# Optimization experiments

Hardware: AMD Instinct MI355X
Metric: run time of the kernel (lower is better)

Reference implementation:

```python
import jax, jax.numpy as jnp
import numpy as np

D_MODEL = 64     # input_dim // 4
D_INNER = 128    # expand * d_model
D_STATE = 16
D_CONV = 4
DT_RANK = 4      # ceil(d_model / 16)
EPS = 1e-5


def layernorm(x, g, b):
    m = x.mean(-1, keepdims=True)
    v = x.var(-1, keepdims=True)
    return (x - m) * jax.lax.rsqrt(v + EPS) * g + b


def mamba(u, W_in, W_conv, b_conv, W_xproj, W_dt, b_dt, A_log, Dp, W_out):
    # u: [B, L, d_model]
    B, L, _ = u.shape
    xz = u @ W_in.T                              # [B, L, 2*d_inner]
    xi, z = xz[..., :D_INNER], xz[..., D_INNER:]
    # depthwise causal conv1d over L
    xp = jnp.pad(xi, ((0, 0), (D_CONV - 1, 0), (0, 0)))
    xc = b_conv + sum(xp[:, k:k + L, :] * W_conv[:, k] for k in range(D_CONV))
    xc = jax.nn.silu(xc)                         # [B, L, d_inner]
    proj = xc @ W_xproj.T                        # [B, L, dt_rank + 2*d_state]
    dtp = proj[..., :DT_RANK]
    Bm = proj[..., DT_RANK:DT_RANK + D_STATE]    # [B, L, d_state]
    Cm = proj[..., DT_RANK + D_STATE:]           # [B, L, d_state]
    dt = jax.nn.softplus(dtp @ W_dt.T + b_dt)    # [B, L, d_inner]
    A = -jnp.exp(A_log)                          # [d_inner, d_state]
    dA = jnp.exp(dt[..., None] * A)              # [B, L, d_inner, d_state]
    dBx = (dt * xc)[..., None] * Bm[:, :, None, :]

    def step(h, t):
        dA_t, dBx_t, C_t = t
        h = dA_t * h + dBx_t                     # [B, d_inner, d_state]
        return h, jnp.einsum('bds,bs->bd', h, C_t)

    h0 = jnp.zeros((B, D_INNER, D_STATE), u.dtype)
    _, ys = jax.lax.scan(step, h0, (dA.transpose(1, 0, 2, 3),
                                    dBx.transpose(1, 0, 2, 3),
                                    Cm.transpose(1, 0, 2)))
    y = ys.transpose(1, 0, 2) + Dp * xc          # [B, L, d_inner]
    y = y * jax.nn.silu(z)
    return y @ W_out.T                           # [B, L, d_model]


def _forward(x, x1, x2, x3, g1, be1, g2, be2, g3, be3, g4, be4, skip_scale,
             W_in, W_conv, b_conv, W_xproj, W_dt, b_dt, A_log, D, W_out):
    Bb, C = x.shape[:2]
    img_dims = x2.shape[2:]
    mparams = (W_in, W_conv, b_conv, W_xproj, W_dt, b_dt, A_log, D, W_out)

    def branch(inp, g, b):
        xf = inp.reshape(Bb, C, -1).transpose(0, 2, 1)   # [B, L, C]
        xn = layernorm(xf, g, b)
        return mamba(xn, *mparams) + skip_scale * xn

    x_mamba = jnp.concatenate([branch(x, g1, be1), branch(x1, g2, be2),
                               branch(x2, g3, be3), branch(x3, g4, be4)], axis=2)
    out = x_mamba.transpose(0, 2, 1).reshape(Bb, 4 * C, *img_dims)
    return out


def setup_inputs():
    key = jax.random.key(0)
    ks = jax.random.split(key, 12)
    f = lambda k, shp, s=1.0: jax.random.normal(k, shp, dtype=jnp.float32) * s
    inp = {
        'x': f(ks[0], (8, 64, 32, 32)),
        'x1': f(ks[1], (8, 64, 32, 32)),
        'x2': f(ks[2], (8, 64, 32, 32)),
        'x3': f(ks[3], (8, 64, 32, 32)),
        'g1': jnp.ones(64), 'be1': jnp.zeros(64),
        'g2': jnp.ones(64), 'be2': jnp.zeros(64),
        'g3': jnp.ones(64), 'be3': jnp.zeros(64),
        'g4': jnp.ones(64), 'be4': jnp.zeros(64),
        'skip_scale': jnp.ones((1,), jnp.float32),
        'W_in': f(ks[4], (2 * D_INNER, D_MODEL), 0.1),
        'W_conv': f(ks[5], (D_INNER, D_CONV), 0.3),
        'b_conv': jnp.zeros(D_INNER),
        'W_xproj': f(ks[6], (DT_RANK + 2 * D_STATE, D_INNER), 0.1),
        'W_dt': f(ks[7], (D_INNER, DT_RANK), 0.1),
        'b_dt': f(ks[8], (D_INNER,), 0.1),
        'A_log': jnp.log(jnp.tile(jnp.arange(1, D_STATE + 1, dtype=jnp.float32), (D_INNER, 1))),
        'D': jnp.ones(D_INNER),
        'W_out': f(ks[9], (D_MODEL, D_INNER), 0.1),
    }
    return inp


def reference(x, x1, x2, x3, g1, be1, g2, be2, g3, be3, g4, be4, skip_scale,
              W_in, W_conv, b_conv, W_xproj, W_dt, b_dt, A_log, D, W_out):
    return _forward(x, x1, x2, x3, g1, be1, g2, be2, g3, be3, g4, be4, skip_scale,
                    W_in, W_conv, b_conv, W_xproj, W_dt, b_dt, A_log, D, W_out)
```

## Files before the change

kernel.cpp:

```cpp
#include <hip/hip_runtime.h>
#include <hip/hip_bf16.h>

#define L2E 1.4426950408889634f
#define LN2 0.6931471805599453f

__device__ __forceinline__ float fexp2(float x) { return __builtin_amdgcn_exp2f(x); }
__device__ __forceinline__ float flog2(float x) { return __builtin_amdgcn_logf(x); }
__device__ __forceinline__ int uniform(int x) { return __builtin_amdgcn_readfirstlane(x); }
__device__ __forceinline__ float sigmoidf_(float v) { return 1.f / (1.f + fexp2(-v * L2E)); }
__device__ __forceinline__ float softplusf_(float t) {
    return (t > 20.f) ? t : LN2 * flog2(1.f + fexp2(t * L2E));
}

constexpr size_t O_M   = 0;
constexpr size_t O_RS  = 32768;
constexpr size_t O_G   = 65536;
constexpr size_t O_Z   = 4259840;
constexpr size_t O_XC  = 8454144;
constexpr size_t O_BM  = 12648448;
constexpr size_t O_CM  = 13172736;
constexpr size_t O_HP  = 13828096;
constexpr size_t O_DT  = 18022400;
constexpr size_t O_DX  = 22216704;

__global__ __launch_bounds__(256) void k1_ln_inproj(
    const float* __restrict__ x0, const float* __restrict__ x1,
    const float* __restrict__ x2, const float* __restrict__ x3,
    const float* __restrict__ win,
    const float* __restrict__ g1, const float* __restrict__ be1,
    const float* __restrict__ g2, const float* __restrict__ be2,
    const float* __restrict__ g3, const float* __restrict__ be3,
    const float* __restrict__ g4, const float* __restrict__ be4,
    float* __restrict__ ws)
{
    __shared__ float sX[64 * 68];
    __shared__ float sW[64 * 68];
    __shared__ float sM[64], sR[64];
    int bid = blockIdx.x;
    int seq = bid >> 4, pb = bid & 15;
    int branch = seq >> 3, b = seq & 7;
    int tid = threadIdx.x;
    int lane = tid & 63;
    int wq = uniform(tid >> 6);
    const float* xin = (branch==0)?x0:(branch==1)?x1:(branch==2)?x2:x3;
    const float* gam = (branch==0)?g1:(branch==1)?g2:(branch==2)?g3:g4;
    const float* bet = (branch==0)?be1:(branch==1)?be2:(branch==2)?be3:be4;
    const float* xb = xin + (size_t)b * 65536;

#pragma unroll
    for (int r = 0; r < 16; ++r) {
        int row = r * 4 + wq;
        sX[row * 68 + lane] = xb[(size_t)row * 1024 + pb * 64 + lane];
    }
    __syncthreads();
    if (tid < 64) {
        float sum = 0.f, sq = 0.f;
#pragma unroll
        for (int c = 0; c < 64; ++c) {
            float v = sX[c * 68 + tid];
            sum += v; sq += v * v;
        }
        float mean = sum * (1.f/64.f);
        float var  = sq * (1.f/64.f) - mean * mean;
        float rs   = rsqrtf(var + 1e-5f);
        sM[tid] = mean; sR[tid] = rs;
        ws[O_M  + (size_t)seq * 1024 + pb * 64 + tid] = mean;
        ws[O_RS + (size_t)seq * 1024 + pb * 64 + tid] = rs;
    }
    __syncthreads();
#pragma unroll
    for (int r = 0; r < 16; ++r) {
        int c = r * 4 + wq;
        float v = sX[c * 68 + lane];
        sX[c * 68 + lane] = (v - sM[lane]) * sR[lane] * gam[c] + bet[c];
    }
    __syncthreads();

    int jt = tid >> 4, pt = tid & 15;
    int p0 = pb * 64 + pt * 4;
    float* xi = ws + O_G + (size_t)seq * 131072;
    float* zz = ws + O_Z + (size_t)seq * 131072;

    for (int jb = 0; jb < 4; ++jb) {
#pragma unroll
        for (int r = 0; r < 16; ++r) {
            int row = r * 4 + wq;
            sW[lane * 68 + row] = win[(size_t)(jb * 64 + row) * 64 + lane];
        }
        __syncthreads();
        float acc[4][4];
#pragma unroll
        for (int i = 0; i < 4; ++i)
#pragma unroll
            for (int j = 0; j < 4; ++j) acc[i][j] = 0.f;
        for (int c = 0; c < 64; ++c) {
            float4 wv = *(const float4*)&sW[c * 68 + jt * 4];
            float4 xv = *(const float4*)&sX[c * 68 + pt * 4];
            float w[4] = {wv.x, wv.y, wv.z, wv.w};
            float x[4] = {xv.x, xv.y, xv.z, xv.w};
#pragma unroll
            for (int i = 0; i < 4; ++i)
#pragma unroll
                for (int j = 0; j < 4; ++j) acc[i][j] += w[i] * x[j];
        }
#pragma unroll
        for (int ji = 0; ji < 4; ++ji) {
            int j = jb * 64 + jt * 4 + ji;
            float4 v = make_float4(acc[ji][0], acc[ji][1], acc[ji][2], acc[ji][3]);
            if (j < 128) *(float4*)&xi[(size_t)j * 1024 + p0] = v;
            else         *(float4*)&zz[(size_t)(j - 128) * 1024 + p0] = v;
        }
        __syncthreads();
    }
}

__global__ __launch_bounds__(256) void k2_conv_proj(
    const float* __restrict__ wconv, const float* __restrict__ bconv,
    const float* __restrict__ wxp,
    const float* __restrict__ wdt, const float* __restrict__ bdt,
    const float* __restrict__ alog,
    float* __restrict__ ws)
{
    __shared__ float buf[17408];
    __shared__ __align__(16) float sDtp4[64 * 4];
    __shared__ float sB5[64 * 20];
    float* sX  = buf;
    float* sWr = buf + 8704;
    float* sDt = buf + 8704;

    int bid = blockIdx.x;
    int seq = bid >> 4, ptile = bid & 15;
    int tid = threadIdx.x;
    int lane = tid & 63;
    int wq = uniform(tid >> 6);
    int p0 = ptile * 64;
    int p  = p0 + lane;
    int j0 = wq * 9;

    const float* xirow = ws + O_G  + (size_t)seq * 131072;
    float*       xcrow = ws + O_XC + (size_t)seq * 131072;

#pragma unroll 4
    for (int r = 0; r < 32; ++r) {
        int d = r * 4 + wq;
        const float* row = xirow + (size_t)d * 1024;
        int gp = p0 - 3 + lane;
        sX[d * 68 + lane] = (gp >= 0) ? row[gp] : 0.f;
        if (lane < 3) sX[d * 68 + 64 + lane] = row[p0 + 61 + lane];
    }
#pragma unroll
    for (int jj = 0; jj < 9; ++jj) {
#pragma unroll
        for (int half = 0; half < 2; ++half) {
            int d = half * 64 + lane;
            sWr[(wq * 128 + d) * 12 + jj] = wxp[(size_t)(j0 + jj) * 128 + d];
        }
    }
    __syncthreads();

#pragma unroll 2
    for (int dd = 0; dd < 32; ++dd) {
        int d = wq * 32 + dd;
        float4 wc = *(const float4*)&wconv[d * 4];
        float v = bconv[d];
        float* rowl = &sX[d * 68];
        v += rowl[lane + 0] * wc.x;
        v += rowl[lane + 1] * wc.y;
        v += rowl[lane + 2] * wc.z;
        v += rowl[lane + 3] * wc.w;
        v = v * sigmoidf_(v);
        xcrow[(size_t)d * 1024 + p] = v;
        rowl[lane + 3] = v;
    }
    __syncthreads();

    float acc[9];
#pragma unroll
    for (int jj = 0; jj < 9; ++jj) acc[jj] = 0.f;
#pragma unroll 4
    for (int d = 0; d < 128; ++d) {
        float xcv = sX[d * 68 + 3 + lane];
        const float* wr = &sWr[(wq * 128 + d) * 12];
        float4 wA = *(const float4*)wr;
        float4 wB = *(const float4*)(wr + 4);
        float  w8 = wr[8];
        acc[0] += wA.x * xcv; acc[1] += wA.y * xcv;
        acc[2] += wA.z * xcv; acc[3] += wA.w * xcv;
        acc[4] += wB.x * xcv; acc[5] += wB.y * xcv;
        acc[6] += wB.z * xcv; acc[7] += wB.w * xcv;
        acc[8] += w8 * xcv;
    }

    float* Bm = ws + O_BM + (size_t)seq * 16384;
    float* Cm = ws + O_CM + (size_t)seq * 16384;
#pragma unroll
    for (int jj = 0; jj < 9; ++jj) {
        int j = j0 + jj;
        if (j < 4) continue;
        float t = acc[jj];
        if (j < 20) { Bm[(size_t)(j - 4) * 1024 + p] = t; sB5[lane * 20 + (j - 4)] = t; }
        else        Cm[(size_t)(j - 20) * 1024 + p] = t;
    }
    if (wq == 0)
        *(float4*)&sDtp4[lane * 4] = make_float4(acc[0], acc[1], acc[2], acc[3]);
    __syncthreads();

    float* dtg = ws + O_DT + (size_t)seq * 131072;
    float* dxg = ws + O_DX + (size_t)seq * 131072;
    float4 qv = *(const float4*)&sDtp4[lane * 4];
#pragma unroll 4
    for (int dd = 0; dd < 32; ++dd) {
        int d = wq * 32 + dd;
        float4 wv = *(const float4*)&wdt[d * 4];
        float t = bdt[d] + qv.x*wv.x + qv.y*wv.y + qv.z*wv.z + qv.w*wv.w;
        float dt = softplusf_(t);
        float xc = sX[d * 68 + 3 + lane];
        float dx = dt * xc;
        dtg[(size_t)d * 1024 + p] = dt;
        dxg[(size_t)d * 1024 + p] = dx;
        sDt[d * 68 + lane] = dt;
        sX [d * 68 + lane] = dx;
    }
    __syncthreads();

    {
        int dA = tid >> 2;
        int dB = dA + 64;
        int s05 = (tid & 3) * 4;
        float a2[8];
        {
            float4 a0 = *(const float4*)(alog + dA * 16 + s05);
            float4 a1 = *(const float4*)(alog + dB * 16 + s05);
            a2[0] = -fexp2(a0.x * L2E) * L2E; a2[1] = -fexp2(a0.y * L2E) * L2E;
            a2[2] = -fexp2(a0.z * L2E) * L2E; a2[3] = -fexp2(a0.w * L2E) * L2E;
            a2[4] = -fexp2(a1.x * L2E) * L2E; a2[5] = -fexp2(a1.y * L2E) * L2E;
            a2[6] = -fexp2(a1.z * L2E) * L2E; a2[7] = -fexp2(a1.w * L2E) * L2E;
        }
        float* hp0 = ws + O_HP + (size_t)(seq * 32 + ptile * 2) * 4096;
#pragma unroll
        for (int cc = 0; cc < 2; ++cc) {
            const float* dtA = &sDt[dA * 68 + cc * 32];
            const float* dtB = &sDt[dB * 68 + cc * 32];
            const float* dxA = &sX [dA * 68 + cc * 32];
            const float* dxB = &sX [dB * 68 + cc * 32];
            float h[8];
#pragma unroll
            for (int i = 0; i < 8; ++i) h[i] = 0.f;
            float sdtA = 0.f, sdtB = 0.f;
            for (int q4 = 0; q4 < 8; ++q4) {
                float4 t0 = *(const float4*)&dtA[q4 * 4];
                float4 t1 = *(const float4*)&dtB[q4 * 4];
                float4 x0 = *(const float4*)&dxA[q4 * 4];
                float4 x1 = *(const float4*)&dxB[q4 * 4];
                float t0a[4] = {t0.x, t0.y, t0.z, t0.w};
                float t1a[4] = {t1.x, t1.y, t1.z, t1.w};
                float x0a[4] = {x0.x, x0.y, x0.z, x0.w};
                float x1a[4] = {x1.x, x1.y, x1.z, x1.w};
#pragma unroll
                for (int k = 0; k < 4; ++k) {
                    int li = q4 * 4 + k;
                    float4 Bv = *(const float4*)&sB5[(cc * 32 + li) * 20 + s05];
                    float bv[4] = {Bv.x, Bv.y, Bv.z, Bv.w};
                    float dt0 = t0a[k], dt1 = t1a[k];
                    float dx0 = x0a[k], dx1 = x1a[k];
                    sdtA += dt0; sdtB += dt1;
#pragma unroll
                    for (int ss = 0; ss < 4; ++ss) {
                        float e0 = fexp2(dt0 * a2[ss]);
                        h[ss] = e0 * h[ss] + dx0 * bv[ss];
                        float e1 = fexp2(dt1 * a2[4 + ss]);
                        h[4 + ss] = e1 * h[4 + ss] + dx1 * bv[ss];
                    }
                }
            }
            float* hp = hp0 + cc * 4096;
            *(float4*)&hp[dA * 16 + s05] = make_float4(
                fexp2(a2[0] * sdtA), fexp2(a2[1] * sdtA),
                fexp2(a2[2] * sdtA), fexp2(a2[3] * sdtA));
            *(float4*)&hp[dB * 16 + s05] = make_float4(
                fexp2(a2[4] * sdtB), fexp2(a2[5] * sdtB),
                fexp2(a2[6] * sdtB), fexp2(a2[7] * sdtB));
            *(float4*)&hp[2048 + dA * 16 + s05] = make_float4(h[0], h[1], h[2], h[3]);
            *(float4*)&hp[2048 + dB * 16 + s05] = make_float4(h[4], h[5], h[6], h[7]);
        }
    }
}

__device__ __forceinline__ void a2_preload(const float* alog, int d0, int s0, float* a2)
{
    float4 a0 = *(const float4*)(alog + d0 * 16 + s0);
    float4 a1 = *(const float4*)(alog + (d0 + 1) * 16 + s0);
    a2[0] = -fexp2(a0.x * L2E) * L2E; a2[1] = -fexp2(a0.y * L2E) * L2E;
    a2[2] = -fexp2(a0.z * L2E) * L2E; a2[3] = -fexp2(a0.w * L2E) * L2E;
    a2[4] = -fexp2(a1.x * L2E) * L2E; a2[5] = -fexp2(a1.y * L2E) * L2E;
    a2[6] = -fexp2(a1.z * L2E) * L2E; a2[7] = -fexp2(a1.w * L2E) * L2E;
}

__global__ __launch_bounds__(256) void k3b_compose(float* __restrict__ ws)
{
    int seq = blockIdx.x >> 3, dg = blockIdx.x & 7;
    int idx = dg * 256 + threadIdx.x;
    float h = 0.f;
    float* hpb = ws + O_HP + (size_t)seq * 32 * 4096;
    float P = hpb[idx];
    float E = hpb[2048 + idx];
    for (int c = 0; c < 32; ++c) {
        float* hp = hpb + (size_t)c * 4096;
        float Pn = 0.f, En = 0.f;
        if (c < 31) { Pn = hp[4096 + idx]; En = hp[4096 + 2048 + idx]; }
        hp[idx] = h;
        h = P * h + E;
        P = Pn; E = En;
    }
}

__global__ __launch_bounds__(256) void k3cd(
    const float* __restrict__ alog,
    const float* __restrict__ x0, const float* __restrict__ x1,
    const float* __restrict__ x2, const float* __restrict__ x3,
    const float* __restrict__ g1, const float* __restrict__ be1,
    const float* __restrict__ g2, const float* __restrict__ be2,
    const float* __restrict__ g3, const float* __restrict__ be3,
    const float* __restrict__ g4, const float* __restrict__ be4,
    const float* __restrict__ dpar, const float* __restrict__ woutp,
    const float* __restrict__ skipp, float* __restrict__ ws,
    float* __restrict__ out)
{
    __shared__ __align__(16) float sY[128 * 36];
    __shared__ __align__(16) float sB[32 * 16];
    __shared__ __align__(16) float sC[32 * 16];
    int bid = blockIdx.x;
    int seq = bid >> 5, ch = bid & 31;
    int branch = seq >> 3, b = seq & 7;
    int lb = ch * 32;
    int tid = threadIdx.x;
    int sq = tid & 3;
    int d0 = (tid >> 2) * 2, s0 = sq * 4;

    float a2[8];
    a2_preload(alog, d0, s0, a2);

    const float* Bmg = ws + O_BM + (size_t)seq * 16384;
    const float* Cmg = ws + O_CM + (size_t)seq * 16384;
    for (int i = tid; i < 512; i += 256) {
        int s = i >> 5, li = i & 31;
        sB[li * 16 + s] = Bmg[(size_t)s * 1024 + lb + li];
        sC[li * 16 + s] = Cmg[(size_t)s * 1024 + lb + li];
    }

    const float* hp = ws + O_HP + (size_t)(seq * 32 + ch) * 4096;
    float4 H0 = *(const float4*)&hp[d0 * 16 + s0];
    float4 H1 = *(const float4*)&hp[(d0 + 1) * 16 + s0];
    float h[8] = {H0.x, H0.y, H0.z, H0.w, H1.x, H1.y, H1.z, H1.w};
    __syncthreads();

    const float* r0t = ws + O_DT + (size_t)seq * 131072 + (size_t)d0 * 1024 + lb;
    const float* r1t = r0t + 1024;
    const float* r0x = ws + O_DX + (size_t)seq * 131072 + (size_t)d0 * 1024 + lb;
    const float* r1x = r0x + 1024;

    for (int q4 = 0; q4 < 8; ++q4) {
        float4 t0 = *(const float4*)&r0t[q4 * 4];
        float4 t1 = *(const float4*)&r1t[q4 * 4];
        float4 x0v = *(const float4*)&r0x[q4 * 4];
        float4 x1v = *(const float4*)&r1x[q4 * 4];
        float t0a[4] = {t0.x, t0.y, t0.z, t0.w};
        float t1a[4] = {t1.x, t1.y, t1.z, t1.w};
        float x0a[4] = {x0v.x, x0v.y, x0v.z, x0v.w};
        float x1a[4] = {x1v.x, x1v.y, x1v.z, x1v.w};
#pragma unroll
        for (int k = 0; k < 4; ++k) {
            int li = q4 * 4 + k;
            float dt0 = t0a[k], dt1 = t1a[k];
            float dx0 = x0a[k], dx1 = x1a[k];
            float4 Bv = *(const float4*)&sB[li * 16 + s0];
            float4 Cv = *(const float4*)&sC[li * 16 + s0];
            float bv[4] = {Bv.x, Bv.y, Bv.z, Bv.w};
            float cv[4] = {Cv.x, Cv.y, Cv.z, Cv.w};
            float acc0 = 0.f, acc1 = 0.f;
#pragma unroll
            for (int ss = 0; ss < 4; ++ss) {
                float e0 = fexp2(dt0 * a2[ss]);
                h[ss] = e0 * h[ss] + dx0 * bv[ss];
                acc0 += h[ss] * cv[ss];
                float e1 = fexp2(dt1 * a2[4 + ss]);
                h[4 + ss] = e1 * h[4 + ss] + dx1 * bv[ss];
                acc1 += h[4 + ss] * cv[ss];
            }
            acc0 += __shfl_xor(acc0, 1); acc0 += __shfl_xor(acc0, 2);
            acc1 += __shfl_xor(acc1, 1); acc1 += __shfl_xor(acc1, 2);
            if (sq == 0) {
                sY[d0 * 36 + li]       = acc0;
                sY[(d0 + 1) * 36 + li] = acc1;
            }
        }
    }
    __syncthreads();

    const float* zzg = ws + O_Z  + (size_t)seq * 131072;
    const float* xcg = ws + O_XC + (size_t)seq * 131072;
    for (int i = tid; i < 4096; i += 256) {
        int d = i >> 5, li = i & 31;
        float zv  = zzg[(size_t)d * 1024 + lb + li];
        float xcv = xcg[(size_t)d * 1024 + lb + li];
        float yv  = sY[d * 36 + li];
        sY[d * 36 + li] = (yv + dpar[d] * xcv) * (zv * sigmoidf_(zv));
    }
    __syncthreads();

    int ctt = tid >> 3;
    int ptq = tid & 7;
    int c0 = ctt * 2;
    const float* w0p = woutp + (size_t)c0 * 128;
    const float* w1p = w0p + 128;
    float acc[2][4];
#pragma unroll
    for (int i = 0; i < 2; ++i)
#pragma unroll
        for (int j = 0; j < 4; ++j) acc[i][j] = 0.f;
    for (int d4 = 0; d4 < 32; ++d4) {
        float4 wa = *(const float4*)&w0p[d4 * 4];
        float4 wb = *(const float4*)&w1p[d4 * 4];
        float waa[4] = {wa.x, wa.y, wa.z, wa.w};
        float wba[4] = {wb.x, wb.y, wb.z, wb.w};
#pragma unroll
        for (int k = 0; k < 4; ++k) {
            int d = d4 * 4 + k;
            float4 gv = *(const float4*)&sY[d * 36 + ptq * 4];
            acc[0][0] += waa[k] * gv.x; acc[0][1] += waa[k] * gv.y;
            acc[0][2] += waa[k] * gv.z; acc[0][3] += waa[k] * gv.w;
            acc[1][0] += wba[k] * gv.x; acc[1][1] += wba[k] * gv.y;
            acc[1][2] += wba[k] * gv.z; acc[1][3] += wba[k] * gv.w;
        }
    }

    const float* xin = (branch==0)?x0:(branch==1)?x1:(branch==2)?x2:x3;
    const float* gam = (branch==0)?g1:(branch==1)?g2:(branch==2)?g3:g4;
    const float* bet = (branch==0)?be1:(branch==1)?be2:(branch==2)?be3:be4;
    const float* xb = xin + (size_t)b * 65536;
    int pp = lb + ptq * 4;
    float skipv = skipp[0];
    float4 m4 = *(const float4*)&ws[O_M  + (size_t)seq * 1024 + pp];
    float4 r4 = *(const float4*)&ws[O_RS + (size_t)seq * 1024 + pp];
    float mm[4] = {m4.x, m4.y, m4.z, m4.w};
    float rr[4] = {r4.x, r4.y, r4.z, r4.w};
#pragma unroll
    for (int ci = 0; ci < 2; ++ci) {
        int c = c0 + ci;
        float4 xv = *(const float4*)&xb[(size_t)c * 1024 + pp];
        float xvv[4] = {xv.x, xv.y, xv.z, xv.w};
        float gc = gam[c], bc = bet[c];
        float o[4];
#pragma unroll
        for (int pi = 0; pi < 4; ++pi) {
            float xn = (xvv[pi] - mm[pi]) * rr[pi] * gc + bc;
            o[pi] = acc[ci][pi] + skipv * xn;
        }
        *(float4*)&out[((size_t)b * 256 + branch * 64 + c) * 1024 + pp] =
            make_float4(o[0], o[1], o[2], o[3]);
    }
}

extern "C" void kernel_launch(void* const* d_in, const int* in_sizes, int n_in,
                              void* d_out, int out_size, void* d_ws, size_t ws_size,
                              hipStream_t stream) {
    float* ws = (float*)d_ws;
    auto f = [&](int i) { return (const float*)d_in[i]; };
    hipLaunchKernelGGL(k1_ln_inproj, dim3(512), dim3(256), 0, stream,
        f(0), f(1), f(2), f(3), f(13),
        f(4), f(5), f(6), f(7), f(8), f(9), f(10), f(11), ws);
    hipLaunchKernelGGL(k2_conv_proj, dim3(512), dim3(256), 0, stream,
        f(14), f(15), f(16), f(17), f(18), f(19), ws);
    hipLaunchKernelGGL(k3b_compose, dim3(256), dim3(256), 0, stream, ws);
    hipLaunchKernelGGL(k3cd, dim3(1024), dim3(256), 0, stream,
        f(19),
        f(0), f(1), f(2), f(3),
        f(4), f(5), f(6), f(7), f(8), f(9), f(10), f(11),
        f(20), f(21), f(12), ws, (float*)d_out);
}
```

Measured before the change: 203.5 us.

## Shrink conv/proj LDS footprint with shuffle-based conv and global dt/dx reads

The conv step of k2_conv_proj now reads each xi row straight from global memory and gets the causal-conv neighbours with wave shuffles plus a 3-element halo, so the padded LDS staging pass goes away. The LDS buffers shrink: sX loses its padding and the weight tile stride drops from 12 to 10. sB5 now reuses the weight area, written after a barrier. The chunk-scan phase reads dt and dx back from global memory, which the same block just wrote, instead of keeping them in LDS. The aim is lower shared-memory use per block, so more blocks fit per CU, at the cost of extra global/L2 traffic and float2 instead of float4 LDS loads.

New measurement: 204.9 us. Within noise of the previous version (+0.6%).

```diff
diff --git a/kernel.cpp b/kernel.cpp
--- a/kernel.cpp
+++ b/kernel.cpp
@@ -121,12 +121,10 @@
     const float* __restrict__ alog,
     float* __restrict__ ws)
 {
-    __shared__ float buf[17408];
+    __shared__ __align__(16) float sX[128 * 64];
+    __shared__ __align__(16) float sWr[4 * 128 * 10];
     __shared__ __align__(16) float sDtp4[64 * 4];
-    __shared__ float sB5[64 * 20];
-    float* sX  = buf;
-    float* sWr = buf + 8704;
-    float* sDt = buf + 8704;
+    float* sB5 = sWr;
 
     int bid = blockIdx.x;
     int seq = bid >> 4, ptile = bid & 15;
@@ -140,37 +138,34 @@
     const float* xirow = ws + O_G  + (size_t)seq * 131072;
     float*       xcrow = ws + O_XC + (size_t)seq * 131072;
 
-#pragma unroll 4
-    for (int r = 0; r < 32; ++r) {
-        int d = r * 4 + wq;
-        const float* row = xirow + (size_t)d * 1024;
-        int gp = p0 - 3 + lane;
-        sX[d * 68 + lane] = (gp >= 0) ? row[gp] : 0.f;
-        if (lane < 3) sX[d * 68 + 64 + lane] = row[p0 + 61 + lane];
-    }
 #pragma unroll
     for (int jj = 0; jj < 9; ++jj) {
 #pragma unroll
         for (int half = 0; half < 2; ++half) {
             int d = half * 64 + lane;
-            sWr[(wq * 128 + d) * 12 + jj] = wxp[(size_t)(j0 + jj) * 128 + d];
-        }
-    }
-    __syncthreads();
-
-#pragma unroll 2
+            sWr[(wq * 128 + d) * 10 + jj] = wxp[(size_t)(j0 + jj) * 128 + d];
+        }
+    }
+
     for (int dd = 0; dd < 32; ++dd) {
         int d = wq * 32 + dd;
+        const float* row = xirow + (size_t)d * 1024;
         float4 wc = *(const float4*)&wconv[d * 4];
-        float v = bconv[d];
-        float* rowl = &sX[d * 68];
-        v += rowl[lane + 0] * wc.x;
-        v += rowl[lane + 1] * wc.y;
-        v += rowl[lane + 2] * wc.z;
-        v += rowl[lane + 3] * wc.w;
-        v = v * sigmoidf_(v);
-        xcrow[(size_t)d * 1024 + p] = v;
-        rowl[lane + 3] = v;
+        float v = row[p];
+        float hv = 0.f;
+        if (lane < 3 && p0 > 0) hv = row[p0 - 3 + lane];
+        float h0 = __shfl(hv, 0), h1 = __shfl(hv, 1), h2 = __shfl(hv, 2);
+        float vm1 = __shfl_up(v, 1); if (lane < 1) vm1 = h2;
+        float vm2 = __shfl_up(v, 2); if (lane < 2) vm2 = (lane == 1) ? h2 : h1;
+        float vm3 = __shfl_up(v, 3); if (lane < 3) vm3 = (lane == 2) ? h2 : (lane == 1) ? h1 : h0;
+        float o = bconv[d];
+        o += vm3 * wc.x;
+        o += vm2 * wc.y;
+        o += vm1 * wc.z;
+        o += v   * wc.w;
+        o = o * sigmoidf_(o);
+        xcrow[(size_t)d * 1024 + p] = o;
+        sX[d * 64 + lane] = o;
     }
     __syncthreads();
 
@@ -179,15 +174,17 @@
     for (int jj = 0; jj < 9; ++jj) acc[jj] = 0.f;
 #pragma unroll 4
     for (int d = 0; d < 128; ++d) {
-        float xcv = sX[d * 68 + 3 + lane];
-        const float* wr = &sWr[(wq * 128 + d) * 12];
-        float4 wA = *(const float4*)wr;
-        float4 wB = *(const float4*)(wr + 4);
-        float  w8 = wr[8];
-        acc[0] += wA.x * xcv; acc[1] += wA.y * xcv;
-        acc[2] += wA.z * xcv; acc[3] += wA.w * xcv;
-        acc[4] += wB.x * xcv; acc[5] += wB.y * xcv;
-        acc[6] += wB.z * xcv; acc[7] += wB.w * xcv;
+        float xcv = sX[d * 64 + lane];
+        const float* wr = &sWr[(wq * 128 + d) * 10];
+        float2 w01 = *(const float2*)(wr);
+        float2 w23 = *(const float2*)(wr + 2);
+        float2 w45 = *(const float2*)(wr + 4);
+        float2 w67 = *(const float2*)(wr + 6);
+        float  w8  = wr[8];
+        acc[0] += w01.x * xcv; acc[1] += w01.y * xcv;
+        acc[2] += w23.x * xcv; acc[3] += w23.y * xcv;
+        acc[4] += w45.x * xcv; acc[5] += w45.y * xcv;
+        acc[6] += w67.x * xcv; acc[7] += w67.y * xcv;
         acc[8] += w8 * xcv;
     }
 
@@ -198,12 +195,18 @@
         int j = j0 + jj;
         if (j < 4) continue;
         float t = acc[jj];
-        if (j < 20) { Bm[(size_t)(j - 4) * 1024 + p] = t; sB5[lane * 20 + (j - 4)] = t; }
+        if (j < 20) Bm[(size_t)(j - 4)  * 1024 + p] = t;
         else        Cm[(size_t)(j - 20) * 1024 + p] = t;
     }
     if (wq == 0)
         *(float4*)&sDtp4[lane * 4] = make_float4(acc[0], acc[1], acc[2], acc[3]);
     __syncthreads();
+
+#pragma unroll
+    for (int jj = 0; jj < 9; ++jj) {
+        int j = j0 + jj;
+        if (j >= 4 && j < 20) sB5[lane * 20 + (j - 4)] = acc[jj];
+    }
 
     float* dtg = ws + O_DT + (size_t)seq * 131072;
     float* dxg = ws + O_DX + (size_t)seq * 131072;
@@ -214,44 +217,40 @@
         float4 wv = *(const float4*)&wdt[d * 4];
         float t = bdt[d] + qv.x*wv.x + qv.y*wv.y + qv.z*wv.z + qv.w*wv.w;
         float dt = softplusf_(t);
-        float xc = sX[d * 68 + 3 + lane];
-        float dx = dt * xc;
+        float dx = dt * sX[d * 64 + lane];
         dtg[(size_t)d * 1024 + p] = dt;
         dxg[(size_t)d * 1024 + p] = dx;
-        sDt[d * 68 + lane] = dt;
-        sX [d * 68 + lane] = dx;
     }
     __syncthreads();
 
     {
         int dA = tid >> 2;
-        int dB = dA + 64;
         int s05 = (tid & 3) * 4;
         float a2[8];
         {
             float4 a0 = *(const float4*)(alog + dA * 16 + s05);
-            float4 a1 = *(const float4*)(alog + dB * 16 + s05);
+            float4 a1 = *(const float4*)(alog + (dA + 64) * 16 + s05);
             a2[0] = -fexp2(a0.x * L2E) * L2E; a2[1] = -fexp2(a0.y * L2E) * L2E;
             a2[2] = -fexp2(a0.z * L2E) * L2E; a2[3] = -fexp2(a0.w * L2E) * L2E;
             a2[4] = -fexp2(a1.x * L2E) * L2E; a2[5] = -fexp2(a1.y * L2E) * L2E;
             a2[6] = -fexp2(a1.z * L2E) * L2E; a2[7] = -fexp2(a1.w * L2E) * L2E;
         }
+        const float* dtA = ws + O_DT + (size_t)seq * 131072 + (size_t)dA * 1024 + p0;
+        const float* dtB = dtA + 65536;
+        const float* dxA = ws + O_DX + (size_t)seq * 131072 + (size_t)dA * 1024 + p0;
+        const float* dxB = dxA + 65536;
         float* hp0 = ws + O_HP + (size_t)(seq * 32 + ptile * 2) * 4096;
 #pragma unroll
         for (int cc = 0; cc < 2; ++cc) {
-            const float* dtA = &sDt[dA * 68 + cc * 32];
-            const float* dtB = &sDt[dB * 68 + cc * 32];
-            const float* dxA = &sX [dA * 68 + cc * 32];
-            const float* dxB = &sX [dB * 68 + cc * 32];
             float h[8];
 #pragma unroll
             for (int i = 0; i < 8; ++i) h[i] = 0.f;
             float sdtA = 0.f, sdtB = 0.f;
             for (int q4 = 0; q4 < 8; ++q4) {
-                float4 t0 = *(const float4*)&dtA[q4 * 4];
-                float4 t1 = *(const float4*)&dtB[q4 * 4];
-                float4 x0 = *(const float4*)&dxA[q4 * 4];
-                float4 x1 = *(const float4*)&dxB[q4 * 4];
+                float4 t0 = *(const float4*)&dtA[cc * 32 + q4 * 4];
+                float4 t1 = *(const float4*)&dtB[cc * 32 + q4 * 4];
+                float4 x0 = *(const float4*)&dxA[cc * 32 + q4 * 4];
+                float4 x1 = *(const float4*)&dxB[cc * 32 + q4 * 4];
                 float t0a[4] = {t0.x, t0.y, t0.z, t0.w};
                 float t1a[4] = {t1.x, t1.y, t1.z, t1.w};
                 float x0a[4] = {x0.x, x0.y, x0.z, x0.w};
@@ -273,15 +272,15 @@
                     }
                 }
             }
-            float* hp = hp0 + cc * 4096;
+            float* hp = hp0 + (size_t)cc * 4096;
             *(float4*)&hp[dA * 16 + s05] = make_float4(
                 fexp2(a2[0] * sdtA), fexp2(a2[1] * sdtA),
                 fexp2(a2[2] * sdtA), fexp2(a2[3] * sdtA));
-            *(float4*)&hp[dB * 16 + s05] = make_float4(
+            *(float4*)&hp[(dA + 64) * 16 + s05] = make_float4(
                 fexp2(a2[4] * sdtB), fexp2(a2[5] * sdtB),
                 fexp2(a2[6] * sdtB), fexp2(a2[7] * sdtB));
-            *(float4*)&hp[2048 + dA * 16 + s05] = make_float4(h[0], h[1], h[2], h[3]);
-            *(float4*)&hp[2048 + dB * 16 + s05] = make_float4(h[4], h[5], h[6], h[7]);
+            *(float4*)&hp[2048 + dA * 16 + s05]        = make_float4(h[0], h[1], h[2], h[3]);
+            *(float4*)&hp[2048 + (dA + 64) * 16 + s05] = make_float4(h[4], h[5], h[6], h[7]);
         }
     }
 }
```
